# Kernel optimization log

Measured on AMD Instinct MI355X. Metric: run time of the kernel, lower is better.

Reference implementation:

```python
import jax, jax.numpy as jnp
import numpy as np

K = 3  # kernel side; ori_col = K*K = 9


def _build_tpcms():
    # order-2: all pairs (i, j), i <= j, over the 9 patch positions
    pairs2 = []
    idx2 = {}
    c = 0
    for i in range(K * K):
        for j in range(i, K * K):
            pairs2.append((i, j))
            idx2[(i, j)] = c
            c += 1
    # order-3: (raw column index i, index of (j, k) in the order-2 tensor), i <= j <= k
    pairs3 = [(i, idx2[(j, k)])
              for i in range(K * K)
              for j in range(i, K * K)
              for k in range(j, K * K)]
    return np.asarray(pairs2, np.int32), np.asarray(pairs3, np.int32)


def setup_inputs() -> dict:
    key = jax.random.key(0)
    x = jax.random.normal(key, (4, 8, 128, 128), dtype=jnp.float32)
    p2, p3 = _build_tpcms()
    return {"x": x, "tpcm2": jnp.asarray(p2), "tpcm3": jnp.asarray(p3)}


def _unfold3x3(x):
    # torch.nn.Unfold(kernel=3, stride=1, pad=1) then view(B, C, 9, L):
    # per channel, the 9 kernel offsets are row-major (kh, kw).
    B, C, H, W = x.shape
    xp = jnp.pad(x, ((0, 0), (0, 0), (1, 1), (1, 1)))
    cols = [xp[:, :, i:i + H, j:j + W] for i in range(K) for j in range(K)]
    return jnp.stack(cols, axis=2).reshape(B, C, K * K, H * W)  # [B, C, 9, L]


def reference(x, tpcm2, tpcm3):
    Col = _unfold3x3(x)                                          # [B, C, 9, L]
    ht2 = Col[:, :, tpcm2[:, 0], :] * Col[:, :, tpcm2[:, 1], :]  # [B, C, 45, L]
    ht3 = Col[:, :, tpcm3[:, 0], :] * ht2[:, :, tpcm3[:, 1], :]  # [B, C, 165, L]
    return jnp.concatenate([ht2, ht3], axis=2)                   # [B, C, 210, L]
```

## Files before the change

### kernel.cpp

```cpp
#include <hip/hip_runtime.h>


#define HH 128
#define WW 128
#define LL (HH * WW)
#define NCH 210

__device__ __forceinline__ constexpr int tri9(int m) { return m * (m + 1) / 2; }

template <bool EDGE>
__device__ __forceinline__ float4 load_tap(const float* __restrict__ xp,
                                           int h, int dh, int dw,
                                           int wq, int w0) {
    const int row = h + dh - 1;
    int off = row * WW + w0 + dw - 1;
    if (dw == 0) off += (wq == 0) ? 1 : 0;
    if (dw == 2) off -= (wq == 31) ? 1 : 0;
    if (EDGE) {
        off = off < 0 ? 0 : off;
        off = off > (LL - 4) ? (LL - 4) : off;
    }
    float4 v = *reinterpret_cast<const float4*>(xp + off);
    if (dw == 0) {
        if (wq == 0)  { v.w = v.z; v.z = v.y; v.y = v.x; v.x = 0.f; }
    }
    if (dw == 2) {
        if (wq == 31) { v.x = v.y; v.y = v.z; v.z = v.w; v.w = 0.f; }
    }
    if (EDGE) {
        if ((unsigned)row >= (unsigned)HH) { v.x = 0.f; v.y = 0.f; v.z = 0.f; v.w = 0.f; }
    }
    return v;
}

template <bool EDGE>
__device__ __forceinline__ void do_row(const float* __restrict__ xp,
                                       float* __restrict__ op,
                                       int h, int wq, int w0,
                                       int dhA, int dwA, int dhB, int dwB,
                                       int dhC, int dwC, bool o3) {
    float4 vb = load_tap<EDGE>(xp, h, dhB, dwB, wq, w0);
    float4 vc = load_tap<EDGE>(xp, h, dhC, dwC, wq, w0);
    float4 t;
    t.x = vb.x * vc.x;
    t.y = vb.y * vc.y;
    t.z = vb.z * vc.z;
    t.w = vb.w * vc.w;
    if (o3) {
        float4 va = load_tap<EDGE>(xp, h, dhA, dwA, wq, w0);
        t.x = va.x * t.x;
        t.y = va.y * t.y;
        t.z = va.z * t.z;
        t.w = va.w * t.w;
    }
    *reinterpret_cast<float4*>(op + h * WW + w0) = t;
}

__global__ __launch_bounds__(256, 4) void hoi_kernel(const float* __restrict__ x,
                                                     float* __restrict__ out) {
    const int ch    = blockIdx.x;
    const int plane = blockIdx.y;

    int A = 0, Bt = 0, Ct = 0;
    bool o3;
    {
        int c = ch;
        if (c < 45) {
            o3 = false;
            int j = 0;
            while (c >= 9 - j) { c -= 9 - j; ++j; }
            Bt = j; Ct = j + c;
        } else {
            o3 = true;
            c -= 45;
            int i = 0;
            while (c >= tri9(9 - i)) { c -= tri9(9 - i); ++i; }
            int j = i;
            while (c >= 9 - j) { c -= 9 - j; ++j; }
            A = i; Bt = j; Ct = j + c;
        }
    }
    const int dhA = A / 3,  dwA = A % 3;
    const int dhB = Bt / 3, dwB = Bt % 3;
    const int dhC = Ct / 3, dwC = Ct % 3;

    const int tid = threadIdx.x;
    const int wq  = tid & 31;
    const int w0  = wq << 2;
    const int hs  = tid >> 5;

    const float* __restrict__ xp = x + (size_t)plane * LL;
    float* __restrict__ op = out + ((size_t)plane * NCH + ch) * LL;

    do_row<true>(xp, op, 0 * 8 + hs, wq, w0, dhA, dwA, dhB, dwB, dhC, dwC, o3);
#pragma unroll
    for (int it = 1; it < 15; ++it)
        do_row<false>(xp, op, it * 8 + hs, wq, w0, dhA, dwA, dhB, dwB, dhC, dwC, o3);
    do_row<true>(xp, op, 15 * 8 + hs, wq, w0, dhA, dwA, dhB, dwB, dhC, dwC, o3);
}

extern "C" void kernel_launch(void* const* d_in, const int* in_sizes, int n_in,
                              void* d_out, int out_size, void* d_ws, size_t ws_size,
                              hipStream_t stream) {
    const float* x = (const float*)d_in[0];
    float* out = (float*)d_out;

    const int nplanes = in_sizes[0] / LL;
    hoi_kernel<<<dim3(NCH, nplanes), 256, 0, stream>>>(x, out);
}
```

Baseline: 504.6 us.

## Compute all 210 channels per pixel quad from registers with nontemporal stores

Instead of one block per output channel re-reading the input taps, each thread now loads its 3x6 neighborhood once into registers and produces all order-2 and order-3 products for its 4 pixels. Each order-2 product is reused for the order-3 products built on it. Stores use nontemporal hints, and the work is split across two grid rows by j range to balance load. The kernel is write-bound at about 440 MB of output, so the gain mainly comes from fewer input reads and cheaper stores. The cost is high register use and scattered per-thread writes across 210 channel planes.

```diff
diff --git a/kernel.cpp b/kernel.cpp
--- a/kernel.cpp
+++ b/kernel.cpp
@@ -6,97 +6,90 @@
 #define LL (HH * WW)
 #define NCH 210
 
-__device__ __forceinline__ constexpr int tri9(int m) { return m * (m + 1) / 2; }
+typedef float v4f __attribute__((ext_vector_type(4)));
 
-template <bool EDGE>
-__device__ __forceinline__ float4 load_tap(const float* __restrict__ xp,
-                                           int h, int dh, int dw,
-                                           int wq, int w0) {
-    const int row = h + dh - 1;
-    int off = row * WW + w0 + dw - 1;
-    if (dw == 0) off += (wq == 0) ? 1 : 0;
-    if (dw == 2) off -= (wq == 31) ? 1 : 0;
-    if (EDGE) {
-        off = off < 0 ? 0 : off;
-        off = off > (LL - 4) ? (LL - 4) : off;
-    }
-    float4 v = *reinterpret_cast<const float4*>(xp + off);
-    if (dw == 0) {
-        if (wq == 0)  { v.w = v.z; v.z = v.y; v.y = v.x; v.x = 0.f; }
-    }
-    if (dw == 2) {
-        if (wq == 31) { v.x = v.y; v.y = v.z; v.z = v.w; v.w = 0.f; }
-    }
-    if (EDGE) {
-        if ((unsigned)row >= (unsigned)HH) { v.x = 0.f; v.y = 0.f; v.z = 0.f; v.w = 0.f; }
-    }
-    return v;
+__host__ __device__ constexpr int ch2_idx(int i, int j) {
+    return i * 9 - (i * (i - 1)) / 2 + (j - i);
+}
+__host__ __device__ constexpr int tri(int m) { return m * (m + 1) / 2; }
+__host__ __device__ constexpr int ch3_idx(int i, int j, int k) {
+    int s = 0;
+    for (int a = 0; a < i; ++a) s += tri(9 - a);
+    for (int b = i; b < j; ++b) s += (9 - b);
+    return 45 + s + (k - j);
 }
 
-template <bool EDGE>
-__device__ __forceinline__ void do_row(const float* __restrict__ xp,
-                                       float* __restrict__ op,
-                                       int h, int wq, int w0,
-                                       int dhA, int dwA, int dhB, int dwB,
-                                       int dhC, int dwC, bool o3) {
-    float4 vb = load_tap<EDGE>(xp, h, dhB, dwB, wq, w0);
-    float4 vc = load_tap<EDGE>(xp, h, dhC, dwC, wq, w0);
-    float4 t;
-    t.x = vb.x * vc.x;
-    t.y = vb.y * vc.y;
-    t.z = vb.z * vc.z;
-    t.w = vb.w * vc.w;
-    if (o3) {
-        float4 va = load_tap<EDGE>(xp, h, dhA, dwA, wq, w0);
-        t.x = va.x * t.x;
-        t.y = va.y * t.y;
-        t.z = va.z * t.z;
-        t.w = va.w * t.w;
+__device__ __forceinline__ void st_nt(float* __restrict__ p, float4 t) {
+    v4f q;
+    q.x = t.x; q.y = t.y; q.z = t.z; q.w = t.w;
+    __builtin_nontemporal_store(q, reinterpret_cast<v4f*>(p));
+}
+
+template <int JLO, int JHI>
+__device__ __forceinline__ void emit(const float4 (&v)[9], float* __restrict__ obase) {
+#pragma unroll
+    for (int j = JLO; j < JHI; ++j) {
+#pragma unroll
+        for (int k = j; k < 9; ++k) {
+            float4 t;
+            t.x = v[j].x * v[k].x;
+            t.y = v[j].y * v[k].y;
+            t.z = v[j].z * v[k].z;
+            t.w = v[j].w * v[k].w;
+            st_nt(obase + ch2_idx(j, k) * LL, t);
+#pragma unroll
+            for (int i = 0; i <= j; ++i) {
+                float4 q;
+                q.x = v[i].x * t.x;
+                q.y = v[i].y * t.y;
+                q.z = v[i].z * t.z;
+                q.w = v[i].w * t.w;
+                st_nt(obase + ch3_idx(i, j, k) * LL, q);
+            }
+        }
     }
-    *reinterpret_cast<float4*>(op + h * WW + w0) = t;
 }
 
 __global__ __launch_bounds__(256, 4) void hoi_kernel(const float* __restrict__ x,
                                                      float* __restrict__ out) {
-    const int ch    = blockIdx.x;
-    const int plane = blockIdx.y;
+    const int tid   = blockIdx.x * 256 + threadIdx.x;
+    const int wq    = tid & 31;
+    const int h     = (tid >> 5) & 127;
+    const int plane = tid >> 12;
+    const int w0    = wq << 2;
 
-    int A = 0, Bt = 0, Ct = 0;
-    bool o3;
-    {
-        int c = ch;
-        if (c < 45) {
-            o3 = false;
-            int j = 0;
-            while (c >= 9 - j) { c -= 9 - j; ++j; }
-            Bt = j; Ct = j + c;
-        } else {
-            o3 = true;
-            c -= 45;
-            int i = 0;
-            while (c >= tri9(9 - i)) { c -= tri9(9 - i); ++i; }
-            int j = i;
-            while (c >= 9 - j) { c -= 9 - j; ++j; }
-            A = i; Bt = j; Ct = j + c;
+    const float* __restrict__ xp = x + (size_t)plane * LL;
+
+    float r[3][6];
+#pragma unroll
+    for (int dh = 0; dh < 3; ++dh) {
+        const int hh = h + dh - 1;
+        const bool hv = (hh >= 0) & (hh < HH);
+#pragma unroll
+        for (int dw = 0; dw < 6; ++dw) {
+            const int ww = w0 + dw - 1;
+            const bool wv = (ww >= 0) & (ww < WW);
+            r[dh][dw] = (hv & wv) ? xp[hh * WW + ww] : 0.0f;
         }
     }
-    const int dhA = A / 3,  dwA = A % 3;
-    const int dhB = Bt / 3, dwB = Bt % 3;
-    const int dhC = Ct / 3, dwC = Ct % 3;
 
-    const int tid = threadIdx.x;
-    const int wq  = tid & 31;
-    const int w0  = wq << 2;
-    const int hs  = tid >> 5;
+    float4 v[9];
+#pragma unroll
+    for (int dh = 0; dh < 3; ++dh) {
+#pragma unroll
+        for (int dw = 0; dw < 3; ++dw) {
+            v[dh * 3 + dw] = make_float4(r[dh][dw], r[dh][dw + 1],
+                                         r[dh][dw + 2], r[dh][dw + 3]);
+        }
+    }
 
-    const float* __restrict__ xp = x + (size_t)plane * LL;
-    float* __restrict__ op = out + ((size_t)plane * NCH + ch) * LL;
+    float* __restrict__ obase = out + (size_t)plane * NCH * LL + h * WW + w0;
 
-    do_row<true>(xp, op, 0 * 8 + hs, wq, w0, dhA, dwA, dhB, dwB, dhC, dwC, o3);
-#pragma unroll
-    for (int it = 1; it < 15; ++it)
-        do_row<false>(xp, op, it * 8 + hs, wq, w0, dhA, dwA, dhB, dwB, dhC, dwC, o3);
-    do_row<true>(xp, op, 15 * 8 + hs, wq, w0, dhA, dwA, dhB, dwB, dhC, dwC, o3);
+    if (blockIdx.y == 0) {
+        emit<0, 4>(v, obase);
+    } else {
+        emit<4, 9>(v, obase);
+    }
 }
 
 extern "C" void kernel_launch(void* const* d_in, const int* in_sizes, int n_in,
@@ -106,5 +99,9 @@
     float* out = (float*)d_out;
 
     const int nplanes = in_sizes[0] / LL;
-    hoi_kernel<<<dim3(NCH, nplanes), 256, 0, stream>>>(x, out);
+    const int total   = nplanes * HH * (WW / 4);
+    const int block   = 256;
+    const int gx      = (total + block - 1) / block;
+
+    hoi_kernel<<<dim3(gx, 2), block, 0, stream>>>(x, out);
 }
```

New measurement: 433.8 us. 1.16x faster.
